# Performance work log

Measured on AMD Instinct MI355X. Metric: run time of the kernel, lower is better.

## Reference

```python
import jax, jax.numpy as jnp
import numpy as np

B = 16384

def _linear_params(key, out_dim, in_dim):
    k1, k2 = jax.random.split(key)
    s = 1.0 / np.sqrt(in_dim)
    W = jax.random.uniform(k1, (out_dim, in_dim), jnp.float32, -s, s)
    b = jax.random.uniform(k2, (out_dim,), jnp.float32, -s, s)
    return W, b

def setup_inputs() -> dict:
    key = jax.random.key(0)
    ks = jax.random.split(key, 6)
    x = jax.random.normal(ks[0], (B, 784), jnp.float32)
    conv_w = jax.random.normal(ks[1], (3, 3), jnp.float32)
    W1, b1 = _linear_params(ks[2], 1024, 26 * 26)
    W2, b2 = _linear_params(ks[3], 512, 1024)
    W3, b3 = _linear_params(ks[4], 256, 512)
    W4, b4 = _linear_params(ks[5], 10, 256)
    return {"x": x, "conv_w": conv_w, "W1": W1, "b1": b1, "W2": W2, "b2": b2,
            "W3": W3, "b3": b3, "W4": W4, "b4": b4}

def reference(x, conv_w, W1, b1, W2, b2, W3, b3, W4, b4):
    b = x.shape[0]
    img = x.reshape(b, 1, 28, 28)                       # NCHW
    kern = conv_w.reshape(1, 1, 3, 3)                   # OIHW; cross-correlation
    y = jax.lax.conv_general_dilated(img, kern, (1, 1), 'VALID')  # [B,1,26,26]
    h = y.reshape(b, 26 * 26)
    h = jax.nn.relu(h @ W1.T + b1)
    h = jax.nn.relu(h @ W2.T + b2)
    h = jax.nn.relu(h @ W3.T + b3)
    return h @ W4.T + b4                                # [B,10] logits
```

## Files before the change

### kernel.cpp

```cpp
#include <hip/hip_runtime.h>
#include <hip/hip_bf16.h>
#include <stdint.h>

#define BDIM 256

typedef __attribute__((ext_vector_type(8))) short short8;
typedef __attribute__((ext_vector_type(4))) float f32x4;

#define AS1 __attribute__((address_space(1)))
#define AS3 __attribute__((address_space(3)))
#define GLL16(g, s) __builtin_amdgcn_global_load_lds((AS1 const void*)(g), (AS3 void*)(s), 16, 0, 0)

__device__ __forceinline__ unsigned short f2bf(float f) {
  union { float f; unsigned u; } v; v.f = f;
  unsigned r = v.u + 0x7fffu + ((v.u >> 16) & 1u);
  return (unsigned short)(r >> 16);
}
__device__ __forceinline__ float bf2f(unsigned short u) {
  union { unsigned u; float f; } v; v.u = ((unsigned)u) << 16;
  return v.f;
}

__global__ __launch_bounds__(BDIM) void cast_pad_w1(const float* __restrict__ w,
                                                    unsigned short* __restrict__ o) {
  int idx = blockIdx.x * BDIM + threadIdx.x;
  if (idx >= 1024 * 704) return;
  int n = idx / 704, k = idx - n * 704;
  float v = (k < 676) ? w[n * 676 + k] : 0.f;
  o[idx] = f2bf(v);
}

__global__ __launch_bounds__(BDIM) void cast_plain(const float* __restrict__ w,
                                                   unsigned short* __restrict__ o, int count) {
  int idx = blockIdx.x * BDIM + threadIdx.x;
  if (idx < count) o[idx] = f2bf(w[idx]);
}

__global__ __launch_bounds__(BDIM) void conv3x3(const float* __restrict__ x,
                                                const float* __restrict__ cw,
                                                unsigned short* __restrict__ h0) {
  __shared__ float xs[784];
  __shared__ float w[9];
  int m = blockIdx.x;
  const float* xr = x + (size_t)m * 784;
  if (threadIdx.x < 9) w[threadIdx.x] = cw[threadIdx.x];
  for (int i = threadIdx.x; i < 784; i += BDIM) xs[i] = xr[i];
  __syncthreads();
  unsigned short* hr = h0 + (size_t)m * 704;
  for (int p = threadIdx.x; p < 704; p += BDIM) {
    float v = 0.f;
    if (p < 676) {
      int r = p / 26, c = p - r * 26;
      const float* xp = &xs[r * 28 + c];
      v = xp[0]  * w[0] + xp[1]  * w[1] + xp[2]  * w[2]
        + xp[28] * w[3] + xp[29] * w[4] + xp[30] * w[5]
        + xp[56] * w[6] + xp[57] * w[7] + xp[58] * w[8];
    }
    hr[p] = f2bf(v);
  }
}

template <int BM, int BN, int WGM, bool RELU>
__global__ __launch_bounds__(BDIM, 4) void gemm_bt5(const unsigned short* __restrict__ A,
                                                    const unsigned short* __restrict__ Wt,
                                                    const float* __restrict__ bias,
                                                    unsigned short* __restrict__ Cb,
                                                    int M, int N, int K) {
  constexpr int WGN = 4 / WGM;
  constexpr int FM = BM / WGM / 16;
  constexpr int FN = BN / WGN / 16;
  constexpr int RA = BM / 64;
  constexpr int RB = BN / 64;
  __shared__ unsigned short lds[2 * (BM + BN) * 32];
  unsigned short* const Asb = lds;
  unsigned short* const Bsb = lds + 2 * BM * 32;

  const int tid = threadIdx.x;
  const int lane = tid & 63;
  const int wid = tid >> 6;

  const int nbm = M / BM, nbc = N / BN;
  const int grid = nbm * nbc;
  const int cpx = grid >> 3;
  const int nid = ((int)blockIdx.x & 7) * cpx + ((int)blockIdx.x >> 3);
  const int brow = (nid / nbc) * BM;
  const int bcol = (nid % nbc) * BN;

  const int srow = tid >> 2;
  const int sslot = (tid & 3) ^ (srow & 3);
  const unsigned short* gA = A + (size_t)(brow + srow) * K + sslot * 8;
  const unsigned short* gB = Wt + (size_t)(bcol + srow) * K + sslot * 8;
  const int sdst = tid * 8;

#define STAGE(buf, kt)                                                        \
  do {                                                                        \
    _Pragma("unroll")                                                         \
    for (int r = 0; r < RA; ++r)                                              \
      GLL16(gA + (size_t)r * 64 * K + (size_t)(kt) * 32,                      \
            Asb + (buf) * BM * 32 + r * 2048 + sdst);                         \
    _Pragma("unroll")                                                         \
    for (int r = 0; r < RB; ++r)                                              \
      GLL16(gB + (size_t)r * 64 * K + (size_t)(kt) * 32,                      \
            Bsb + (buf) * BN * 32 + r * 2048 + sdst);                         \
  } while (0)

  f32x4 acc[FM][FN] = {};
  const int fr = lane & 15;
  const int h = lane >> 4;
  const int fx = fr & 3;
  const int abase = (wid / WGN) * (FM * 16);
  const int bbase = (wid % WGN) * (FN * 16);
  const int slot = (h ^ fx) << 3;

  const int nk = K >> 5;
  STAGE(0, 0);
  __syncthreads();
  int cur = 0;
  for (int kt = 0; kt < nk; ++kt) {
    if (kt + 1 < nk) STAGE(cur ^ 1, kt + 1);
    const unsigned short* As0 = Asb + cur * BM * 32;
    const unsigned short* Bs0 = Bsb + cur * BN * 32;
    short8 af[FM], bf[FN];
#pragma unroll
    for (int m = 0; m < FM; ++m)
      af[m] = *(const short8*)&As0[(abase + m * 16 + fr) * 32 + slot];
#pragma unroll
    for (int n = 0; n < FN; ++n)
      bf[n] = *(const short8*)&Bs0[(bbase + n * 16 + fr) * 32 + slot];
#pragma unroll
    for (int m = 0; m < FM; ++m)
#pragma unroll
      for (int n = 0; n < FN; ++n)
        acc[m][n] = __builtin_amdgcn_mfma_f32_16x16x32_bf16(af[m], bf[n], acc[m][n], 0, 0, 0);
    __syncthreads();
    cur ^= 1;
  }
#undef STAGE

  unsigned short* const scr = lds;
  const int lrow0 = abase + (h << 2);
  const int lcol0 = bbase + fr;
#pragma unroll
  for (int n = 0; n < FN; ++n) {
    const int col = lcol0 + n * 16;
    const float bv = bias[bcol + col];
#pragma unroll
    for (int m = 0; m < FM; ++m) {
#pragma unroll
      for (int j = 0; j < 4; ++j) {
        const int row = lrow0 + m * 16 + j;
        float v = acc[m][n][j] + bv;
        if (RELU) v = v > 0.f ? v : 0.f;
        scr[(row * BN + col) ^ ((row & 12) << 2)] = f2bf(v);
      }
    }
  }
  __syncthreads();
  constexpr int CPR = BN / 8;
  constexpr int TOT = BM * CPR;
#pragma unroll 2
  for (int i = tid; i < TOT; i += BDIM) {
    const int row = i / CPR, c = i % CPR;
    const int cs = c ^ ((row & 12) >> 1);
    short8 vv = *(const short8*)&scr[row * BN + cs * 8];
    *(short8*)(Cb + (size_t)(brow + row) * N + bcol + c * 8) = vv;
  }
}

__global__ __launch_bounds__(BDIM) void fc10(const unsigned short* __restrict__ h3,
                                             const float* __restrict__ W4,
                                             const float* __restrict__ b4,
                                             float* __restrict__ out) {
  int lane = threadIdx.x & 63;
  int wid = threadIdx.x >> 6;
  int m = blockIdx.x * 4 + wid;
  const unsigned short* hr = h3 + (size_t)m * 256 + lane * 4;
  uint64_t hv = *(const uint64_t*)hr;
  float e0 = bf2f((unsigned short)hv), e1 = bf2f((unsigned short)(hv >> 16));
  float e2 = bf2f((unsigned short)(hv >> 32)), e3 = bf2f((unsigned short)(hv >> 48));
#pragma unroll
  for (int n = 0; n < 10; ++n) {
    const float4 wv = *(const float4*)(W4 + n * 256 + lane * 4);
    float s = e0 * wv.x + e1 * wv.y + e2 * wv.z + e3 * wv.w;
#pragma unroll
    for (int off = 32; off > 0; off >>= 1) s += __shfl_xor(s, off);
    if (lane == n) out[(size_t)m * 10 + n] = s + b4[n];
  }
}

extern "C" void kernel_launch(void* const* d_in, const int* in_sizes, int n_in,
                              void* d_out, int out_size, void* d_ws, size_t ws_size,
                              hipStream_t stream) {
  const float* x  = (const float*)d_in[0];
  const float* cw = (const float*)d_in[1];
  const float* W1 = (const float*)d_in[2];
  const float* b1 = (const float*)d_in[3];
  const float* W2 = (const float*)d_in[4];
  const float* b2 = (const float*)d_in[5];
  const float* W3 = (const float*)d_in[6];
  const float* b3 = (const float*)d_in[7];
  const float* W4 = (const float*)d_in[8];
  const float* b4 = (const float*)d_in[9];
  float* out = (float*)d_out;

  char* ws = (char*)d_ws;
  unsigned short* h0  = (unsigned short*)(ws);
  unsigned short* h1  = (unsigned short*)(ws + 23068672);
  unsigned short* W1b = (unsigned short*)(ws + 23068672 + 33554432);
  unsigned short* W2b = W1b + 1024 * 704;
  unsigned short* W3b = W2b + 512 * 1024;
  unsigned short* h2  = h0;
  unsigned short* h3  = h1;

  cast_pad_w1<<<2816, BDIM, 0, stream>>>(W1, W1b);
  cast_plain<<<2048, BDIM, 0, stream>>>(W2, W2b, 512 * 1024);
  cast_plain<<<512, BDIM, 0, stream>>>(W3, W3b, 256 * 512);
  conv3x3<<<16384, BDIM, 0, stream>>>(x, cw, h0);

  gemm_bt5<128, 128, 2, true><<<(16384 / 128) * (1024 / 128), BDIM, 0, stream>>>(
      h0, W1b, b1, h1, 16384, 1024, 704);
  gemm_bt5<64, 128, 1, true><<<(16384 / 64) * (512 / 128), BDIM, 0, stream>>>(
      h1, W2b, b2, h2, 16384, 512, 1024);
  gemm_bt5<64, 64, 2, true><<<(16384 / 64) * (256 / 64), BDIM, 0, stream>>>(
      h2, W3b, b3, h3, 16384, 256, 512);
  fc10<<<16384 / 4, BDIM, 0, stream>>>(h3, W4, b4, out);
}
```

Before: 123.5 us.

## Load GEMM weight fragments directly into registers and stage only activations in LDS

The GEMM kernel is restructured so each wave owns a column slice of the tile for all rows. It loads its weight fragments straight from global memory into registers, double-buffered across k-steps, while only the activation tile goes through LDS via async global-to-LDS loads. Explicit vmcnt waits, raw s_barrier, sched barriers and setprio around the MFMA block replace __syncthreads. Tile shapes for the second and third GEMMs grow to 128 rows and occupancy drops to 3 blocks. This cuts LDS traffic and footprint for the B operand, at the cost of uncoalesced per-lane global weight loads, more registers, and a brittle hand-written wait count.

Result: slower. 136.7 us (+10.7%).

```diff
diff --git a/kernel.cpp b/kernel.cpp
--- a/kernel.cpp
+++ b/kernel.cpp
@@ -19,6 +19,20 @@
 __device__ __forceinline__ float bf2f(unsigned short u) {
   union { unsigned u; float f; } v; v.u = ((unsigned)u) << 16;
   return v.f;
+}
+
+template <int N> __device__ __forceinline__ void vmwait() {
+  static_assert(N >= 0 && N <= 8, "unsupported vmcnt");
+  if constexpr (N == 8)      asm volatile("s_waitcnt vmcnt(8)" ::: "memory");
+  else if constexpr (N == 7) asm volatile("s_waitcnt vmcnt(7)" ::: "memory");
+  else if constexpr (N == 6) asm volatile("s_waitcnt vmcnt(6)" ::: "memory");
+  else if constexpr (N == 5) asm volatile("s_waitcnt vmcnt(5)" ::: "memory");
+  else if constexpr (N == 4) asm volatile("s_waitcnt vmcnt(4)" ::: "memory");
+  else if constexpr (N == 3) asm volatile("s_waitcnt vmcnt(3)" ::: "memory");
+  else if constexpr (N == 2) asm volatile("s_waitcnt vmcnt(2)" ::: "memory");
+  else if constexpr (N == 1) asm volatile("s_waitcnt vmcnt(1)" ::: "memory");
+  else                       asm volatile("s_waitcnt vmcnt(0)" ::: "memory");
+  __builtin_amdgcn_sched_barrier(0);
 }
 
 __global__ __launch_bounds__(BDIM) void cast_pad_w1(const float* __restrict__ w,
@@ -60,20 +74,17 @@
   }
 }
 
-template <int BM, int BN, int WGM, bool RELU>
-__global__ __launch_bounds__(BDIM, 4) void gemm_bt5(const unsigned short* __restrict__ A,
-                                                    const unsigned short* __restrict__ Wt,
-                                                    const float* __restrict__ bias,
-                                                    unsigned short* __restrict__ Cb,
-                                                    int M, int N, int K) {
-  constexpr int WGN = 4 / WGM;
-  constexpr int FM = BM / WGM / 16;
-  constexpr int FN = BN / WGN / 16;
+template <int BM, int BN, bool RELU>
+__global__ __launch_bounds__(BDIM, 3) void gemm_bd(const unsigned short* __restrict__ A,
+                                                   const unsigned short* __restrict__ Wt,
+                                                   const float* __restrict__ bias,
+                                                   unsigned short* __restrict__ Cb,
+                                                   int M, int N, int K) {
+  constexpr int FM = BM / 16;
+  constexpr int FN = BN / 64;
   constexpr int RA = BM / 64;
-  constexpr int RB = BN / 64;
-  __shared__ unsigned short lds[2 * (BM + BN) * 32];
-  unsigned short* const Asb = lds;
-  unsigned short* const Bsb = lds + 2 * BM * 32;
+  constexpr int LDSE = (2 * BM * 32 > BM * BN) ? 2 * BM * 32 : BM * BN;
+  __shared__ unsigned short lds[LDSE];
 
   const int tid = threadIdx.x;
   const int lane = tid & 63;
@@ -87,58 +98,72 @@
   const int bcol = (nid % nbc) * BN;
 
   const int srow = tid >> 2;
-  const int sslot = (tid & 3) ^ (srow & 3);
+  const int sslot = (tid & 3) ^ ((srow >> 1) & 3);
   const unsigned short* gA = A + (size_t)(brow + srow) * K + sslot * 8;
-  const unsigned short* gB = Wt + (size_t)(bcol + srow) * K + sslot * 8;
   const int sdst = tid * 8;
 
-#define STAGE(buf, kt)                                                        \
-  do {                                                                        \
-    _Pragma("unroll")                                                         \
+#define STAGE_A(buf, kt)                                                      \
+  do { _Pragma("unroll")                                                      \
     for (int r = 0; r < RA; ++r)                                              \
       GLL16(gA + (size_t)r * 64 * K + (size_t)(kt) * 32,                      \
-            Asb + (buf) * BM * 32 + r * 2048 + sdst);                         \
-    _Pragma("unroll")                                                         \
-    for (int r = 0; r < RB; ++r)                                              \
-      GLL16(gB + (size_t)r * 64 * K + (size_t)(kt) * 32,                      \
-            Bsb + (buf) * BN * 32 + r * 2048 + sdst);                         \
+            lds + (buf) * BM * 32 + r * 2048 + sdst);                         \
   } while (0)
 
   f32x4 acc[FM][FN] = {};
   const int fr = lane & 15;
   const int h = lane >> 4;
-  const int fx = fr & 3;
-  const int abase = (wid / WGN) * (FM * 16);
-  const int bbase = (wid % WGN) * (FN * 16);
-  const int slot = (h ^ fx) << 3;
+  const int fx = (fr >> 1) & 3;
+  const int bbase = wid * (FN * 16);
+
+  const unsigned short* gB = Wt + (size_t)(bcol + bbase + fr) * K + h * 8;
 
   const int nk = K >> 5;
-  STAGE(0, 0);
-  __syncthreads();
+  short8 bc[FN], bn[FN];
+#define LOADB(dst, kt)                                                        \
+  do { _Pragma("unroll")                                                      \
+    for (int n = 0; n < FN; ++n)                                              \
+      dst[n] = *(const short8*)(gB + (size_t)(n * 16) * K + (size_t)(kt) * 32); \
+  } while (0)
+
+  STAGE_A(0, 0);
+  LOADB(bc, 0);
+  vmwait<0>();
+  __builtin_amdgcn_s_barrier();
+  __builtin_amdgcn_sched_barrier(0);
+
   int cur = 0;
   for (int kt = 0; kt < nk; ++kt) {
-    if (kt + 1 < nk) STAGE(cur ^ 1, kt + 1);
-    const unsigned short* As0 = Asb + cur * BM * 32;
-    const unsigned short* Bs0 = Bsb + cur * BN * 32;
-    short8 af[FM], bf[FN];
+    if (kt + 1 < nk) {
+      STAGE_A(cur ^ 1, kt + 1);
+      LOADB(bn, kt + 1);
+    }
+    __builtin_amdgcn_sched_barrier(0);
+    const unsigned short* As0 = lds + cur * BM * 32;
+    short8 af[FM];
 #pragma unroll
     for (int m = 0; m < FM; ++m)
-      af[m] = *(const short8*)&As0[(abase + m * 16 + fr) * 32 + slot];
-#pragma unroll
-    for (int n = 0; n < FN; ++n)
-      bf[n] = *(const short8*)&Bs0[(bbase + n * 16 + fr) * 32 + slot];
+      af[m] = *(const short8*)&As0[(m * 16 + fr) * 32 + ((h ^ fx) << 3)];
+    __builtin_amdgcn_s_setprio(1);
 #pragma unroll
     for (int m = 0; m < FM; ++m)
 #pragma unroll
       for (int n = 0; n < FN; ++n)
-        acc[m][n] = __builtin_amdgcn_mfma_f32_16x16x32_bf16(af[m], bf[n], acc[m][n], 0, 0, 0);
-    __syncthreads();
+        acc[m][n] = __builtin_amdgcn_mfma_f32_16x16x32_bf16(af[m], bc[n], acc[m][n], 0, 0, 0);
+    __builtin_amdgcn_s_setprio(0);
+    __builtin_amdgcn_sched_barrier(0);
+    if (kt + 1 < nk) vmwait<FN>();
+    else             vmwait<0>();
+    __builtin_amdgcn_s_barrier();
+    __builtin_amdgcn_sched_barrier(0);
+#pragma unroll
+    for (int n = 0; n < FN; ++n) bc[n] = bn[n];
     cur ^= 1;
   }
-#undef STAGE
+#undef STAGE_A
+#undef LOADB
 
   unsigned short* const scr = lds;
-  const int lrow0 = abase + (h << 2);
+  const int lrow0 = h << 2;
   const int lcol0 = bbase + fr;
 #pragma unroll
   for (int n = 0; n < FN; ++n) {
@@ -217,11 +242,11 @@
   cast_plain<<<512, BDIM, 0, stream>>>(W3, W3b, 256 * 512);
   conv3x3<<<16384, BDIM, 0, stream>>>(x, cw, h0);
 
-  gemm_bt5<128, 128, 2, true><<<(16384 / 128) * (1024 / 128), BDIM, 0, stream>>>(
+  gemm_bd<128, 128, true><<<(16384 / 128) * (1024 / 128), BDIM, 0, stream>>>(
       h0, W1b, b1, h1, 16384, 1024, 704);
-  gemm_bt5<64, 128, 1, true><<<(16384 / 64) * (512 / 128), BDIM, 0, stream>>>(
+  gemm_bd<128, 128, true><<<(16384 / 128) * (512 / 128), BDIM, 0, stream>>>(
       h1, W2b, b2, h2, 16384, 512, 1024);
-  gemm_bt5<64, 64, 2, true><<<(16384 / 64) * (256 / 64), BDIM, 0, stream>>>(
+  gemm_bd<128, 64, true><<<(16384 / 128) * (256 / 64), BDIM, 0, stream>>>(
       h2, W3b, b3, h3, 16384, 256, 512);
   fc10<<<16384 / 4, BDIM, 0, stream>>>(h3, W4, b4, out);
 }
```
